# Performance work log

Measured on AMD Instinct MI355X. Metric: run time of the kernel, lower is better.

## Reference

```python
import jax, jax.numpy as jnp
import numpy as np

NUM_USER = 10000
NUM_ITEM = 30000
N = NUM_USER + NUM_ITEM          # total nodes
DIM = 64                          # dim_E == dim_C
E = 500000                        # user-item interactions
NUM_ROUTING = 3
ALPHA_THR = 0.5
NEG_SLOPE_ATTN = 0.2              # GAT attention leaky slope
NEG_SLOPE_ACT = 0.01              # F.leaky_relu_ default


def l2norm(x, eps=1e-12):
    n = jnp.linalg.norm(x, axis=-1, keepdims=True)
    return x / jnp.maximum(n, eps)


def seg_softmax(score, seg):
    # numerically-stable softmax over edges grouped by destination node
    m = jax.ops.segment_max(score, seg, num_segments=N)
    e = jnp.exp(score - m[seg])
    s = jax.ops.segment_sum(e, seg, num_segments=N)
    return e / (s[seg] + 1e-16)


def gat_ori(x, W, src, dst):
    # GATConv_ori: dot-product attention, softmax per destination, scatter-add
    h = x @ W                                     # [N, C]
    score = jax.nn.leaky_relu(jnp.sum(h[dst] * h[src], -1), NEG_SLOPE_ATTN)
    alpha = seg_softmax(score, dst)               # [2E]
    return jax.ops.segment_sum(alpha[:, None] * h[src], dst, num_segments=N)


def gat_pre(x, y, z, W, src, dst):
    # GATConv_pre: primary-modality attention modulated by cross-modal gate (reattn)
    hx = x @ W
    sx = jnp.sum(hx[dst] * hx[src], -1)
    sy = jnp.sum(y[dst] * y[src], -1)
    sz = jnp.sum(z[dst] * z[src], -1)
    alpha = seg_softmax(jax.nn.leaky_relu(sx, NEG_SLOPE_ATTN), dst)
    gate = jax.nn.sigmoid(0.5 * (sy + sz))
    alpha = jnp.where(gate > ALPHA_THR, alpha * gate, alpha)
    return jax.ops.segment_sum(alpha[:, None] * hx[src], dst, num_segments=N)


def cgcn(pref, feat, pref2, feat2, pref3, feat3, src, dst, Wpre, Wori):
    x = jnp.concatenate([pref, feat], 0)
    y = jnp.concatenate([pref2, feat2], 0)
    z = jnp.concatenate([pref3, feat3], 0)
    x = l2norm(gat_pre(x, y, z, Wpre, src, dst))
    for _ in range(NUM_ROUTING):
        x = l2norm(x + gat_ori(x, Wori, src, dst))
    return x


def gcn_conv(x, W, src, dst):
    return jax.ops.segment_sum((x @ W)[src], dst, num_segments=N)


def real_gcn(id_emb, Wg, src, dst):
    x = l2norm(id_emb)
    h1 = jax.nn.leaky_relu(gcn_conv(x, Wg[0], src, dst), NEG_SLOPE_ACT)
    h2 = jax.nn.leaky_relu(gcn_conv(h1, Wg[1], src, dst), NEG_SLOPE_ACT)
    h3 = gcn_conv(h1, Wg[2], src, dst)
    return x + h1 + h2 + h3


def setup_inputs() -> dict:
    key = jax.random.key(0)
    ks = jax.random.split(key, 16)
    users = jax.random.randint(ks[0], (E,), 0, NUM_USER)
    items = jax.random.randint(ks[1], (E,), NUM_USER, N)
    edge_index = jnp.stack([users, items]).astype(jnp.int64)
    s = 0.05
    return {
        'edge_index': edge_index,
        'v_feat': jax.random.normal(ks[2], (NUM_ITEM, 128), jnp.float32),
        'a_feat': jax.random.normal(ks[3], (NUM_ITEM, 128), jnp.float32),
        't_feat': jax.random.normal(ks[4], (NUM_ITEM, 100), jnp.float32),
        'pref_v': jax.random.normal(ks[5], (NUM_USER, DIM), jnp.float32) * s,
        'pref_a': jax.random.normal(ks[6], (NUM_USER, DIM), jnp.float32) * s,
        'pref_t': jax.random.normal(ks[7], (NUM_USER, DIM), jnp.float32) * s,
        'mlp_v_w': jax.random.normal(ks[8], (DIM, 128), jnp.float32) * s,
        'mlp_v_b': jnp.zeros((DIM,), jnp.float32),
        'mlp_a_w': jax.random.normal(ks[9], (DIM, 128), jnp.float32) * s,
        'mlp_a_b': jnp.zeros((DIM,), jnp.float32),
        'mlp_t_w': jax.random.normal(ks[10], (DIM, 100), jnp.float32) * s,
        'mlp_t_b': jnp.zeros((DIM,), jnp.float32),
        'pre_w': jax.random.normal(ks[11], (3, DIM, DIM), jnp.float32) * s,
        'ori_w': jax.random.normal(ks[12], (3, DIM, DIM), jnp.float32) * s,
        'gcn_w': jax.random.normal(ks[13], (3, DIM, DIM), jnp.float32) * s,
        'id_embedding': jax.random.normal(ks[14], (N, DIM), jnp.float32) * s,
    }


def reference(edge_index, v_feat, a_feat, t_feat, pref_v, pref_a, pref_t,
              mlp_v_w, mlp_v_b, mlp_a_w, mlp_a_b, mlp_t_w, mlp_t_b,
              pre_w, ori_w, gcn_w, id_embedding):
    # symmetrize edges (cat with flipped); no self-loops possible (bipartite)
    src = jnp.concatenate([edge_index[0], edge_index[1]])
    dst = jnp.concatenate([edge_index[1], edge_index[0]])

    fv = l2norm(jax.nn.leaky_relu(v_feat @ mlp_v_w.T + mlp_v_b, NEG_SLOPE_ACT))
    fa = l2norm(jax.nn.leaky_relu(a_feat @ mlp_a_w.T + mlp_a_b, NEG_SLOPE_ACT))
    ft = l2norm(jax.nn.leaky_relu(t_feat @ mlp_t_w.T + mlp_t_b, NEG_SLOPE_ACT))
    pv, pa, pt = l2norm(pref_v), l2norm(pref_a), l2norm(pref_t)

    v_rep = cgcn(pv, fv, pa, fa, pt, ft, src, dst, pre_w[0], ori_w[0])
    a_rep = cgcn(pa, fa, pv, fv, pt, ft, src, dst, pre_w[1], ori_w[1])
    t_rep = cgcn(pt, ft, pa, fa, pv, fv, src, dst, pre_w[2], ori_w[2])
    id_rep = real_gcn(id_embedding, gcn_w, src, dst)

    return jnp.concatenate([id_rep, v_rep, a_rep, t_rep], axis=1)  # [N, 4*DIM]
```

## Files before the change

kernel.cpp:

```cpp
#include <hip/hip_runtime.h>
#include <hip/hip_fp16.h>
#include <math.h>

#define NUSER 10000
#define NITEM 30000
#define NN    40000
#define DD    64
#define PLANE ((size_t)NN * DD)

typedef _Float16 hv2 __attribute__((ext_vector_type(2)));
union U2H { unsigned u; hv2 v; __half2 hh; };

#if defined(__has_builtin)
#if __has_builtin(__builtin_amdgcn_fdot2)
#define HAS_FDOT2 1
#endif
#endif

__device__ __forceinline__ float fdot2u(unsigned a, unsigned b, float c) {
#ifdef HAS_FDOT2
    U2H x, y;
    x.u = a;
    y.u = b;
    return __builtin_amdgcn_fdot2(x.v, y.v, c, false);
// ... 53 lines not shown
    __shared__ int wsh[4];
    int b = blockIdx.x, tid = threadIdx.x;
    int base = b * chunk, end = min(n, base + chunk);
    int s = 0;
    for (int i = base + tid; i < end; i += 256) s += cnt[i];
#pragma unroll
    for (int o = 32; o > 0; o >>= 1) s += __shfl_xor(s, o, 64);
    if ((tid & 63) == 0) wsh[tid >> 6] = s;
    __syncthreads();
    if (tid == 0) bsum[b] = wsh[0] + wsh[1] + wsh[2] + wsh[3];
}

__global__ void k_bscan(int* bsum, int nb, int* rp_end) {
    int lane = threadIdx.x;
    int v = (lane < nb) ? bsum[lane] : 0;
    int orig = v;
#pragma unroll
    for (int o = 1; o < 64; o <<= 1) {
        int y = __shfl_up(v, o, 64);
        if (lane >= o) v += y;
    }
    if (lane < nb) bsum[lane] = v - orig;
    if (lane == 63) *rp_end = v;
}

__global__ void k_apply(const int* __restrict__ cnt, const int* __restrict__ boff,
                        int* __restrict__ rp, int n, int chunk) {
    __shared__ int buf[256];
    __shared__ int csh;
    int b = blockIdx.x, tid = threadIdx.x;
    int base = b * chunk, end = min(n, base + chunk);
    int carry = boff[b];
    for (int t0 = base; t0 < end; t0 += 256) {
        int i = t0 + tid;
        int v = (i < end) ? cnt[i] : 0;
        int x = v;
        buf[tid] = x;
        __syncthreads();
        for (int o = 1; o < 256; o <<= 1) {
            int y = (tid >= o) ? buf[tid - o] : 0;
            __syncthreads();
            x += y;
            buf[tid] = x;
            __syncthreads();
        }
        if (i < end) rp[i] = carry + x - v;
        __syncthreads();
        if (tid == 255) csh = carry + x;
        __syncthreads();
        carry = csh;
    }
}

__global__ void k_scatter(const int* ei, int E2, int E, const int* rp, int* fill, int* col) {
    int i = blockIdx.x * blockDim.x + threadIdx.x;
    if (i >= E2) return;
    int j = (i < E) ? i : i - E;
    int s = (i < E) ? ei[j] : ei[E + j];
    int d = (i < E) ? ei[E + j] : ei[j];
    int pos = rp[d] + atomicAdd(&fill[d], 1);
    col[pos] = s;
}

__global__ void k_prep_pref(const float* __restrict__ pv, const float* __restrict__ pa,
                            const float* __restrict__ pt, __half* __restrict__ M) {
    int t = blockIdx.x * blockDim.x + threadIdx.x;
    int w = t >> 6, lane = t & 63, nw = (gridDim.x * blockDim.x) >> 6;
    for (int r = w; r < NUSER; r += nw) {
        float a = pv[(size_t)r * DD + lane];
        float b = pa[(size_t)r * DD + lane];
        float c = pt[(size_t)r * DD + lane];
        float sa = a * a, sb = b * b, sc = c * c;
#pragma unroll
        for (int o = 32; o > 0; o >>= 1) {
            sa += __shfl_xor(sa, o, 64);
            sb += __shfl_xor(sb, o, 64);
            sc += __shfl_xor(sc, o, 64);
        }
        size_t base = (size_t)r * 3 * DD + lane;
        M[base] = __float2half(a / fmaxf(sqrtf(sa), 1e-12f));
        M[base + DD] = __float2half(b / fmaxf(sqrtf(sb), 1e-12f));
        M[base + 2 * DD] = __float2half(c / fmaxf(sqrtf(sc), 1e-12f));
    }
}

template <int K>
__global__ void k_mlp(const float* __restrict__ feat, const float* __restrict__ W,
                      const float* __restrict__ bias, __half* __restrict__ M, int mo) {
    constexpr int K4 = K / 4;
    __shared__ float4 Wl[K4][DD];
    __shared__ float4 rbuf[4][2][K4];
    int t = threadIdx.x, wib = t >> 6, lane = t & 63;
    for (int i = t; i < DD * K4; i += 256) {
        int c = i / K4, k4 = i - c * K4;
        Wl[k4][c] = *(const float4*)(W + (size_t)c * K + k4 * 4);
    }
    __syncthreads();
    float b = bias[lane];
    const int stride = gridDim.x * 4;
    int r = blockIdx.x * 4 + wib;
    float4 v = {0.f, 0.f, 0.f, 0.f};
    if (r < NITEM && lane < K4) v = *(const float4*)(feat + (size_t)r * K + lane * 4);
    int cur = 0;
    for (; r < NITEM; r += stride) {
        if (lane < K4) rbuf[wib][cur][lane] = v;
        int rn = r + stride;
        if (rn < NITEM && lane < K4) v = *(const float4*)(feat + (size_t)rn * K + lane * 4);
        asm volatile("s_waitcnt lgkmcnt(0)" ::: "memory");
        float acc = b;
#pragma unroll
        for (int k4 = 0; k4 < K4; k4++) {
            float4 x4 = rbuf[wib][cur][k4];
            float4 w4 = Wl[k4][lane];
            acc += x4.x * w4.x + x4.y * w4.y + x4.z * w4.z + x4.w * w4.w;
        }
        float h = acc > 0.f ? acc : 0.01f * acc;
        float n = sqrtf(wsum(h * h));
        M[((size_t)(NUSER + r) * 3 + mo) * DD + lane] = __float2half(h / fmaxf(n, 1e-12f));
        cur ^= 1;
    }
}

__global__ void k_gemm_h3(const __half* __restrict__ x3, const float* __restrict__ W3,
                          __half* __restrict__ o3) {
    __shared__ float rowbuf[4][DD];
    int mo = blockIdx.y;
    const float* W = W3 + (size_t)mo * 4096;
    int t = threadIdx.x, wib = t >> 6, lane = t & 63;
    float Wc[DD];
#pragma unroll
    for (int k = 0; k < DD; k++) Wc[k] = W[k * DD + lane];
    for (int r = blockIdx.x * 4 + wib; r < NN; r += gridDim.x * 4) {
        size_t idx = ((size_t)r * 3 + mo) * DD + lane;
        rowbuf[wib][lane] = __half2float(x3[idx]);
        asm volatile("s_waitcnt lgkmcnt(0)" ::: "memory");
        float acc = 0.f;
#pragma unroll
        for (int k4 = 0; k4 < DD / 4; k4++) {
            float4 xq = *(const float4*)&rowbuf[wib][k4 * 4];
            acc += xq.x * Wc[k4 * 4] + xq.y * Wc[k4 * 4 + 1] + xq.z * Wc[k4 * 4 + 2] +
                   xq.w * Wc[k4 * 4 + 3];
        }
        o3[idx] = __float2half(acc);
    }
}

__global__ void k_gemm_f2(const float* __restrict__ x, const float* __restrict__ W2,
                          __half* __restrict__ o2) {
    __shared__ float rowbuf[4][DD];
    int mo = blockIdx.y;
    const float* W = W2 + (size_t)mo * 4096;
    int t = threadIdx.x, wib = t >> 6, lane = t & 63;
    float Wc[DD];
#pragma unroll
    for (int k = 0; k < DD; k++) Wc[k] = W[k * DD + lane];
    for (int r = blockIdx.x * 4 + wib; r < NN; r += gridDim.x * 4) {
        rowbuf[wib][lane] = x[(size_t)r * DD + lane];
        asm volatile("s_waitcnt lgkmcnt(0)" ::: "memory");
        float acc = 0.f;
#pragma unroll
        for (int k4 = 0; k4 < DD / 4; k4++) {
            float4 xq = *(const float4*)&rowbuf[wib][k4 * 4];
            acc += xq.x * Wc[k4 * 4] + xq.y * Wc[k4 * 4 + 1] + xq.z * Wc[k4 * 4 + 2] +
                   xq.w * Wc[k4 * 4 + 3];
        }
        o2[((size_t)r * 2 + mo) * DD + lane] = __float2half(acc);
    }
}

__global__ void k_gemm_id(const float* __restrict__ x, const float* __restrict__ W,
                          __half* __restrict__ hout, float* __restrict__ xnorm) {
    __shared__ float rowbuf[4][DD];
    int t = threadIdx.x, wib = t >> 6, lane = t & 63;
    float Wc[DD];
#pragma unroll
    for (int k = 0; k < DD; k++) Wc[k] = W[k * DD + lane];
    for (int r = blockIdx.x * 4 + wib; r < NN; r += gridDim.x * 4) {
        float xv = x[(size_t)r * DD + lane];
        float n = sqrtf(wsum(xv * xv));
        xv /= fmaxf(n, 1e-12f);
        xnorm[(size_t)r * DD + lane] = xv;
        rowbuf[wib][lane] = xv;
        asm volatile("s_waitcnt lgkmcnt(0)" ::: "memory");
        float acc = 0.f;
#pragma unroll
        for (int k4 = 0; k4 < DD / 4; k4++) {
            float4 xq = *(const float4*)&rowbuf[wib][k4 * 4];
            acc += xq.x * Wc[k4 * 4] + xq.y * Wc[k4 * 4 + 1] + xq.z * Wc[k4 * 4 + 2] +
                   xq.w * Wc[k4 * 4 + 3];
        }
        hout[(size_t)r * DD + lane] = __float2half(acc);
    }
}

__device__ __forceinline__ float gatef(float ssum) {
    float gate = 1.f / (1.f + __expf(-0.5f * ssum));
    return gate > 0.5f ? gate : 1.f;
}

__global__ void k_edgedot3(const __half* __restrict__ M, const int* __restrict__ rp,
                           const int* __restrict__ col, __half* __restrict__ gf4) {
    int t = blockIdx.x * blockDim.x + threadIdx.x;
    int wv = t >> 6, lane = t & 63, nw = (gridDim.x * blockDim.x) >> 6;
    int g = lane >> 3, q = lane & 7;
    for (int w0 = wv; w0 < NN; w0 += nw) {
        int n = nodeperm(w0);
        int e0 = rp[n], e1 = rp[n + 1];
        if (e0 == e1) continue;
        const uint4* trow = (const uint4*)(M + (size_t)n * 192);
        uint4 tv = trow[q], ta = trow[q + 8], tt = trow[q + 16];
        for (int eb = e0 + g; eb < e1; eb += 8) {
            int sn = col[eb];
            const uint4* srow = (const uint4*)(M + (size_t)sn * 192);
            uint4 sv = srow[q], sa = srow[q + 8], st = srow[q + 16];
            float dv = dot8(tv, sv), da = dot8(ta, sa), dt = dot8(tt, st);
            dv = qsum8(dv);
            da = qsum8(da);
            dt = qsum8(dt);
            if (q == 0) {
                U2H p01, p2;
                p01.hh = __floats2half2_rn(gatef(da + dt), gatef(dv + dt));
                p2.hh = __floats2half2_rn(gatef(da + dv), 0.f);
                *(uint2*)(gf4 + (size_t)eb * 4) = make_uint2(p01.u, p2.u);
            }
        }
    }
}

__global__ void k_gat_pre3(const __half* __restrict__ h3, const __half* __restrict__ gf4,
                           const int* __restrict__ rp, const int* __restrict__ col,
                           __half* __restrict__ x3h) {
    int t = blockIdx.x * blockDim.x + threadIdx.x;
    int wv = t >> 6, lane = t & 63, nw = (gridDim.x * blockDim.x) >> 6;
    int g = lane >> 3, q = lane & 7;
    const __half2 z = __floats2half2_rn(0.f, 0.f);
    for (int w0 = wv; w0 < NN; w0 += nw) {
        int n = nodeperm(w0);
        int e0 = rp[n], e1 = rp[n + 1];
        const uint4* hrow = (const uint4*)(h3 + (size_t)n * 192);
        uint4 hd0 = hrow[q], hd1 = hrow[q + 8], hd2 = hrow[q + 16];
        float s0 = 0.f, s1 = 0.f, s2 = 0.f;
        __half2 a0[4] = {z, z, z, z}, a1[4] = {z, z, z, z}, a2[4] = {z, z, z, z};
        for (int eb = e0 + g; eb < e1; eb += 8) {
            int sn = col[eb];
            const uint4* srow = (const uint4*)(h3 + (size_t)sn * 192);
            uint4 v0 = srow[q], v1 = srow[q + 8], v2 = srow[q + 16];
            uint2 gv = *(const uint2*)(gf4 + (size_t)eb * 4);
            float d0 = dot8(hd0, v0), d1 = dot8(hd1, v1), d2 = dot8(hd2, v2);
            d0 = qsum8(d0);
            d1 = qsum8(d1);
            d2 = qsum8(d2);
            float2 g01 = __half22float2(uh(gv.x));
            float g2 = __half22float2(uh(gv.y)).x;
            float sc0 = d0 > 0.f ? d0 : 0.2f * d0;
            float sc1 = d1 > 0.f ? d1 : 0.2f * d1;
            float sc2 = d2 > 0.f ? d2 : 0.2f * d2;
            float p0 = __expf(sc0), p1 = __expf(sc1), p2 = __expf(sc2);
            s0 += p0;
            s1 += p1;
            s2 += p2;
            __half2 ph0 = __float2half2_rn(p0 * g01.x);
            __half2 ph1 = __float2half2_rn(p1 * g01.y);
            __half2 ph2 = __float2half2_rn(p2 * g2);
            a0[0] = __hfma2(ph0, uh(v0.x), a0[0]);
            a0[1] = __hfma2(ph0, uh(v0.y), a0[1]);
            a0[2] = __hfma2(ph0, uh(v0.z), a0[2]);
            a0[3] = __hfma2(ph0, uh(v0.w), a0[3]);
            a1[0] = __hfma2(ph1, uh(v1.x), a1[0]);
            a1[1] = __hfma2(ph1, uh(v1.y), a1[1]);
            a1[2] = __hfma2(ph1, uh(v1.z), a1[2]);
            a1[3] = __hfma2(ph1, uh(v1.w), a1[3]);
            a2[0] = __hfma2(ph2, uh(v2.x), a2[0]);
            a2[1] = __hfma2(ph2, uh(v2.y), a2[1]);
            a2[2] = __hfma2(ph2, uh(v2.z), a2[2]);
            a2[3] = __hfma2(ph2, uh(v2.w), a2[3]);
        }
        s0 = gsum8(s0);
        s1 = gsum8(s1);
        s2 = gsum8(s2);
#pragma unroll
        for (int j = 0; j < 4; j++) {
            a0[j] = h2rx(h2rx(h2rx(a0[j], 8), 16), 32);
            a1[j] = h2rx(h2rx(h2rx(a1[j], 8), 16), 32);
            a2[j] = h2rx(h2rx(h2rx(a2[j], 8), 16), 32);
        }
        float i0 = 1.f / (s0 + 1e-16f), i1 = 1.f / (s1 + 1e-16f), i2 = 1.f / (s2 + 1e-16f);
        float o0[8], o1[8], o2[8];
#pragma unroll
        for (int j = 0; j < 4; j++) {
            float2 f0 = __half22float2(a0[j]);
            float2 f1 = __half22float2(a1[j]);
            float2 f2 = __half22float2(a2[j]);
            o0[2 * j] = f0.x * i0;
            o0[2 * j + 1] = f0.y * i0;
            o1[2 * j] = f1.x * i1;
            o1[2 * j + 1] = f1.y * i1;
            o2[2 * j] = f2.x * i2;
            o2[2 * j + 1] = f2.y * i2;
        }
        float n0 = 0.f, n1 = 0.f, n2 = 0.f;
#pragma unroll
        for (int k = 0; k < 8; k++) {
            n0 += o0[k] * o0[k];
            n1 += o1[k] * o1[k];
            n2 += o2[k] * o2[k];
        }
        n0 = qsum8(n0);
        n1 = qsum8(n1);
        n2 = qsum8(n2);
        float r0 = 1.f / fmaxf(sqrtf(n0), 1e-12f);
        float r1 = 1.f / fmaxf(sqrtf(n1), 1e-12f);
        float r2 = 1.f / fmaxf(sqrtf(n2), 1e-12f);
        if (g == 0) {
            uint4* orow = (uint4*)(x3h + (size_t)n * 192);
            uint4 w0_, w1_, w2_;
            w0_.x = hu(__floats2half2_rn(o0[0] * r0, o0[1] * r0));
            w0_.y = hu(__floats2half2_rn(o0[2] * r0, o0[3] * r0));
            w0_.z = hu(__floats2half2_rn(o0[4] * r0, o0[5] * r0));
            w0_.w = hu(__floats2half2_rn(o0[6] * r0, o0[7] * r0));
            w1_.x = hu(__floats2half2_rn(o1[0] * r1, o1[1] * r1));
            w1_.y = hu(__floats2half2_rn(o1[2] * r1, o1[3] * r1));
            w1_.z = hu(__floats2half2_rn(o1[4] * r1, o1[5] * r1));
            w1_.w = hu(__floats2half2_rn(o1[6] * r1, o1[7] * r1));
            w2_.x = hu(__floats2half2_rn(o2[0] * r2, o2[1] * r2));
            w2_.y = hu(__floats2half2_rn(o2[2] * r2, o2[3] * r2));
            w2_.z = hu(__floats2half2_rn(o2[4] * r2, o2[5] * r2));
            w2_.w = hu(__floats2half2_rn(o2[6] * r2, o2[7] * r2));
            orow[q] = w0_;
            orow[q + 8] = w1_;
            orow[q + 16] = w2_;
        }
    }
}

__global__ void k_gat_ori3(const __half* __restrict__ h3, const __half* __restrict__ x3h,
                           const int* __restrict__ rp, const int* __restrict__ col,
                           __half* __restrict__ xout, float* __restrict__ fout) {
    int t = blockIdx.x * blockDim.x + threadIdx.x;
    int wv = t >> 6, lane = t & 63, nw = (gridDim.x * blockDim.x) >> 6;
    int g = lane >> 3, q = lane & 7;
    const __half2 z = __floats2half2_rn(0.f, 0.f);
    for (int w0 = wv; w0 < NN; w0 += nw) {
        int n = nodeperm(w0);
        int e0 = rp[n], e1 = rp[n + 1];
        const uint4* hrow = (const uint4*)(h3 + (size_t)n * 192);
        uint4 hd0 = hrow[q], hd1 = hrow[q + 8], hd2 = hrow[q + 16];
        float s0 = 0.f, s1 = 0.f, s2 = 0.f;
        __half2 a0[4] = {z, z, z, z}, a1[4] = {z, z, z, z}, a2[4] = {z, z, z, z};
        for (int eb = e0 + g; eb < e1; eb += 8) {
            int sn = col[eb];
            const uint4* srow = (const uint4*)(h3 + (size_t)sn * 192);
            uint4 v0 = srow[q], v1 = srow[q + 8], v2 = srow[q + 16];
            float d0 = dot8(hd0, v0), d1 = dot8(hd1, v1), d2 = dot8(hd2, v2);
            d0 = qsum8(d0);
            d1 = qsum8(d1);
            d2 = qsum8(d2);
            float sc0 = d0 > 0.f ? d0 : 0.2f * d0;
            float sc1 = d1 > 0.f ? d1 : 0.2f * d1;
            float sc2 = d2 > 0.f ? d2 : 0.2f * d2;
            float p0 = __expf(sc0), p1 = __expf(sc1), p2 = __expf(sc2);
            s0 += p0;
            s1 += p1;
            s2 += p2;
            __half2 ph0 = __float2half2_rn(p0);
            __half2 ph1 = __float2half2_rn(p1);
            __half2 ph2 = __float2half2_rn(p2);
            a0[0] = __hfma2(ph0, uh(v0.x), a0[0]);
            a0[1] = __hfma2(ph0, uh(v0.y), a0[1]);
            a0[2] = __hfma2(ph0, uh(v0.z), a0[2]);
            a0[3] = __hfma2(ph0, uh(v0.w), a0[3]);
            a1[0] = __hfma2(ph1, uh(v1.x), a1[0]);
            a1[1] = __hfma2(ph1, uh(v1.y), a1[1]);
            a1[2] = __hfma2(ph1, uh(v1.z), a1[2]);
            a1[3] = __hfma2(ph1, uh(v1.w), a1[3]);
            a2[0] = __hfma2(ph2, uh(v2.x), a2[0]);
            a2[1] = __hfma2(ph2, uh(v2.y), a2[1]);
            a2[2] = __hfma2(ph2, uh(v2.z), a2[2]);
            a2[3] = __hfma2(ph2, uh(v2.w), a2[3]);
        }
        s0 = gsum8(s0);
        s1 = gsum8(s1);
        s2 = gsum8(s2);
#pragma unroll
        for (int j = 0; j < 4; j++) {
            a0[j] = h2rx(h2rx(h2rx(a0[j], 8), 16), 32);
            a1[j] = h2rx(h2rx(h2rx(a1[j], 8), 16), 32);
            a2[j] = h2rx(h2rx(h2rx(a2[j], 8), 16), 32);
        }
        float i0 = 1.f / (s0 + 1e-16f), i1 = 1.f / (s1 + 1e-16f), i2 = 1.f / (s2 + 1e-16f);
        const uint4* xrow = (const uint4*)(x3h + (size_t)n * 192);
        uint4 xr0 = xrow[q], xr1 = xrow[q + 8], xr2 = xrow[q + 16];
        float o0[8], o1[8], o2[8];
#pragma unroll
        for (int j = 0; j < 4; j++) {
            float2 f0 = __half22float2(a0[j]);
            float2 f1 = __half22float2(a1[j]);
            float2 f2 = __half22float2(a2[j]);
            float2 xf0 = __half22float2(uh(j == 0 ? xr0.x : j == 1 ? xr0.y : j == 2 ? xr0.z : xr0.w));
            float2 xf1 = __half22float2(uh(j == 0 ? xr1.x : j == 1 ? xr1.y : j == 2 ? xr1.z : xr1.w));
            float2 xf2 = __half22float2(uh(j == 0 ? xr2.x : j == 1 ? xr2.y : j == 2 ? xr2.z : xr2.w));
            o0[2 * j] = xf0.x + f0.x * i0;
            o0[2 * j + 1] = xf0.y + f0.y * i0;
            o1[2 * j] = xf1.x + f1.x * i1;
            o1[2 * j + 1] = xf1.y + f1.y * i1;
            o2[2 * j] = xf2.x + f2.x * i2;
            o2[2 * j + 1] = xf2.y + f2.y * i2;
        }
        float n0 = 0.f, n1 = 0.f, n2 = 0.f;
#pragma unroll
        for (int k = 0; k < 8; k++) {
            n0 += o0[k] * o0[k];
            n1 += o1[k] * o1[k];
            n2 += o2[k] * o2[k];
        }
        n0 = qsum8(n0);
        n1 = qsum8(n1);
        n2 = qsum8(n2);
        float r0 = 1.f / fmaxf(sqrtf(n0), 1e-12f);
        float r1 = 1.f / fmaxf(sqrtf(n1), 1e-12f);
        float r2 = 1.f / fmaxf(sqrtf(n2), 1e-12f);
        if (g == 0) {
            if (fout) {
                float* ob = fout + (size_t)n * 256 + 64 + q * 8;
                float4 wa, wb;
                wa = make_float4(o0[0] * r0, o0[1] * r0, o0[2] * r0, o0[3] * r0);
                wb = make_float4(o0[4] * r0, o0[5] * r0, o0[6] * r0, o0[7] * r0);
                *(float4*)(ob) = wa;
                *(float4*)(ob + 4) = wb;
                wa = make_float4(o1[0] * r1, o1[1] * r1, o1[2] * r1, o1[3] * r1);
                wb = make_float4(o1[4] * r1, o1[5] * r1, o1[6] * r1, o1[7] * r1);
                *(float4*)(ob + 64) = wa;
                *(float4*)(ob + 68) = wb;
                wa = make_float4(o2[0] * r2, o2[1] * r2, o2[2] * r2, o2[3] * r2);
                wb = make_float4(o2[4] * r2, o2[5] * r2, o2[6] * r2, o2[7] * r2);
                *(float4*)(ob + 128) = wa;
                *(float4*)(ob + 132) = wb;
            } else {
                uint4* orow = (uint4*)(xout + (size_t)n * 192);
                uint4 w0_, w1_, w2_;
                w0_.x = hu(__floats2half2_rn(o0[0] * r0, o0[1] * r0));
                w0_.y = hu(__floats2half2_rn(o0[2] * r0, o0[3] * r0));
                w0_.z = hu(__floats2half2_rn(o0[4] * r0, o0[5] * r0));
                w0_.w = hu(__floats2half2_rn(o0[6] * r0, o0[7] * r0));
                w1_.x = hu(__floats2half2_rn(o1[0] * r1, o1[1] * r1));
                w1_.y = hu(__floats2half2_rn(o1[2] * r1, o1[3] * r1));
                w1_.z = hu(__floats2half2_rn(o1[4] * r1, o1[5] * r1));
                w1_.w = hu(__floats2half2_rn(o1[6] * r1, o1[7] * r1));
                w2_.x = hu(__floats2half2_rn(o2[0] * r2, o2[1] * r2));
                w2_.y = hu(__floats2half2_rn(o2[2] * r2, o2[3] * r2));
                w2_.z = hu(__floats2half2_rn(o2[4] * r2, o2[5] * r2));
                w2_.w = hu(__floats2half2_rn(o2[6] * r2, o2[7] * r2));
                orow[q] = w0_;
                orow[q + 8] = w1_;
                orow[q + 16] = w2_;
            }
        }
    }
}

__global__ void k_gcn1(const __half* __restrict__ h, const int* __restrict__ rp,
                       const int* __restrict__ col, float* __restrict__ out) {
    int t = blockIdx.x * blockDim.x + threadIdx.x;
    int wv = t >> 6, lane = t & 63, nw = (gridDim.x * blockDim.x) >> 6;
    int g = lane >> 3, q = lane & 7;
    const __half2 z = __floats2half2_rn(0.f, 0.f);
    for (int w0 = wv; w0 < NN; w0 += nw) {
        int n = nodeperm(w0);
        int e0 = rp[n], e1 = rp[n + 1];
        __half2 a[4] = {z, z, z, z};
        for (int eb = e0 + g; eb < e1; eb += 8) {
            int sn = col[eb];
            uint4 v = ((const uint4*)(h + (size_t)sn * DD))[q];
            a[0] = __hadd2(a[0], uh(v.x));
            a[1] = __hadd2(a[1], uh(v.y));
            a[2] = __hadd2(a[2], uh(v.z));
            a[3] = __hadd2(a[3], uh(v.w));
        }
#pragma unroll
        for (int j = 0; j < 4; j++) a[j] = h2rx(h2rx(h2rx(a[j], 8), 16), 32);
        if (g == 0) {
            float o[8];
#pragma unroll
            for (int j = 0; j < 4; j++) {
                float2 f = __half22float2(a[j]);
                o[2 * j] = f.x > 0.f ? f.x : 0.01f * f.x;
                o[2 * j + 1] = f.y > 0.f ? f.y : 0.01f * f.y;
            }
            float* ob = out + (size_t)n * DD + q * 8;
            *(float4*)(ob) = make_float4(o[0], o[1], o[2], o[3]);
            *(float4*)(ob + 4) = make_float4(o[4], o[5], o[6], o[7]);
        }
    }
}

__global__ void k_gcn_final2(const __half* __restrict__ gp, const int* __restrict__ rp,
                             const int* __restrict__ col, const float* __restrict__ x0,
                             const float* __restrict__ h1, float* __restrict__ out) {
    int t = blockIdx.x * blockDim.x + threadIdx.x;
    int wv = t >> 6, lane = t & 63, nw = (gridDim.x * blockDim.x) >> 6;
    int g = lane >> 3, q = lane & 7;
    const __half2 z = __floats2half2_rn(0.f, 0.f);
    for (int w0 = wv; w0 < NN; w0 += nw) {
        int n = nodeperm(w0);
        int e0 = rp[n], e1 = rp[n + 1];
        __half2 aA[4] = {z, z, z, z}, aB[4] = {z, z, z, z};
        for (int eb = e0 + g; eb < e1; eb += 8) {
            int sn = col[eb];
// ... 22 lines not shown
#pragma unroll
            for (int j = 0; j < 4; j++) {
                float2 fA = __half22float2(aA[j]);
                float2 fB = __half22float2(aB[j]);
                float h2x = fA.x > 0.f ? fA.x : 0.01f * fA.x;
                float h2y = fA.y > 0.f ? fA.y : 0.01f * fA.y;
                o[2 * j] = h2x + fB.x;
                o[2 * j + 1] = h2y + fB.y;
            }
            float* ob = out + (size_t)n * 256 + q * 8;
            *(float4*)(ob) = make_float4(o[0] + v0a.x + v1a.x, o[1] + v0a.y + v1a.y,
                                         o[2] + v0a.z + v1a.z, o[3] + v0a.w + v1a.w);
            *(float4*)(ob + 4) = make_float4(o[4] + v0b.x + v1b.x, o[5] + v0b.y + v1b.y,
                                             o[6] + v0b.z + v1b.z, o[7] + v0b.w + v1b.w);
        }
    }
}

extern "C" void kernel_launch(void* const* d_in, const int* in_sizes, int n_in,
                              void* d_out, int out_size, void* d_ws, size_t ws_size,
                              hipStream_t stream) {
    const int* ei       = (const int*)d_in[0];
    const float* v_feat = (const float*)d_in[1];
    const float* a_feat = (const float*)d_in[2];
    const float* t_feat = (const float*)d_in[3];
    const float* pref_v = (const float*)d_in[4];
    const float* pref_a = (const float*)d_in[5];
    const float* pref_t = (const float*)d_in[6];
    const float* mlp_v_w = (const float*)d_in[7];
    const float* mlp_v_b = (const float*)d_in[8];
    const float* mlp_a_w = (const float*)d_in[9];
    const float* mlp_a_b = (const float*)d_in[10];
    const float* mlp_t_w = (const float*)d_in[11];
    const float* mlp_t_b = (const float*)d_in[12];
    const float* pre_w  = (const float*)d_in[13];
    const float* ori_w  = (const float*)d_in[14];
    const float* gcn_w  = (const float*)d_in[15];
    const float* id_emb = (const float*)d_in[16];
    float* out = (float*)d_out;

    const int E2 = in_sizes[0];
    const int E  = E2 / 2;

    char* w = (char*)d_ws;
    auto alloc = [&](size_t bytes) -> void* {
        void* p = (void*)w;
        w += (bytes + 255) & ~(size_t)255;
        return p;
    };
    int* cnt  = (int*)alloc((size_t)NN * 4);
    int* rp   = (int*)alloc((size_t)(NN + 1) * 4);
    int* bsum = (int*)alloc(256);
    int* col  = (int*)alloc((size_t)E2 * 4);
    __half* Mh3  = (__half*)alloc(3 * PLANE * 2);
    __half* hb3h = (__half*)alloc(3 * PLANE * 2);
    __half* x3h  = (__half*)alloc(3 * PLANE * 2);
    __half* gf4  = (__half*)alloc((size_t)E2 * 4 * 2);
    float* x0f = (float*)alloc(PLANE * 4);
    float* h1f = (float*)alloc(PLANE * 4);

    __half* g1 = hb3h;
    __half* gpair = hb3h + PLANE;

    const int NBLK = 64, CHUNK = (NN + NBLK - 1) / NBLK;
    hipMemsetAsync(cnt, 0, (size_t)NN * 4, stream);
    k_hist<<<(E2 + 255) / 256, 256, 0, stream>>>(ei, E2, E, cnt);
    k_bsum<<<NBLK, 256, 0, stream>>>(cnt, bsum, NN, CHUNK);
    k_bscan<<<1, 64, 0, stream>>>(bsum, NBLK, rp + NN);
    k_apply<<<NBLK, 256, 0, stream>>>(cnt, bsum, rp, NN, CHUNK);
    hipMemsetAsync(cnt, 0, (size_t)NN * 4, stream);
    k_scatter<<<(E2 + 255) / 256, 256, 0, stream>>>(ei, E2, E, rp, cnt, col);

    k_prep_pref<<<640, 256, 0, stream>>>(pref_v, pref_a, pref_t, Mh3);
    k_mlp<128><<<1024, 256, 0, stream>>>(v_feat, mlp_v_w, mlp_v_b, Mh3, 0);
    k_mlp<128><<<1024, 256, 0, stream>>>(a_feat, mlp_a_w, mlp_a_b, Mh3, 1);
    k_mlp<100><<<1024, 256, 0, stream>>>(t_feat, mlp_t_w, mlp_t_b, Mh3, 2);

    const int GB = (NN + 3) / 4;

    k_edgedot3<<<GB, 256, 0, stream>>>(Mh3, rp, col, gf4);

    dim3 g3(1280, 3);
    k_gemm_h3<<<g3, 256, 0, stream>>>(Mh3, pre_w, hb3h);
    k_gat_pre3<<<GB, 256, 0, stream>>>(hb3h, gf4, rp, col, x3h);
    for (int it = 0; it < 3; it++) {
        k_gemm_h3<<<g3, 256, 0, stream>>>(x3h, ori_w, hb3h);
        if (it < 2)
            k_gat_ori3<<<GB, 256, 0, stream>>>(hb3h, x3h, rp, col, x3h, nullptr);
        else
            k_gat_ori3<<<GB, 256, 0, stream>>>(hb3h, x3h, rp, col, nullptr, out);
    }

    k_gemm_id<<<1280, 256, 0, stream>>>(id_emb, gcn_w, g1, x0f);
    k_gcn1<<<GB, 256, 0, stream>>>(g1, rp, col, h1f);
    dim3 g2(1280, 2);
    k_gemm_f2<<<g2, 256, 0, stream>>>(h1f, gcn_w + 4096, gpair);
    k_gcn_final2<<<GB, 256, 0, stream>>>(gpair, rp, col, x0f, h1f, out);
}
```

Before: 661.5 us.

## Split modality-interleaved node features into planes and run GAT per modality

Changes the feature layout from one interleaved [node][3][64] array to three separate planes. The fused three-modality GAT kernels become single-modality kernels launched once per plane, which shrinks the per-row gather so each plane's working set fits better in cache. The edge dot products are now computed only once per undirected edge, from user nodes, using a new edge-permutation array; they are combined into gates and then expanded to CSR order. The cost is more kernel launches, extra passes over the gate arrays, and no longer sharing col and index loads across modalities.

```diff
diff --git a/kernel.cpp b/kernel.cpp
--- a/kernel.cpp
+++ b/kernel.cpp
@@ -129,7 +129,8 @@
     }
 }
 
-__global__ void k_scatter(const int* ei, int E2, int E, const int* rp, int* fill, int* col) {
+__global__ void k_scatter(const int* ei, int E2, int E, const int* rp, int* fill, int* col,
+                          int* ep) {
     int i = blockIdx.x * blockDim.x + threadIdx.x;
     if (i >= E2) return;
     int j = (i < E) ? i : i - E;
@@ -137,6 +138,7 @@
     int d = (i < E) ? ei[E + j] : ei[j];
     int pos = rp[d] + atomicAdd(&fill[d], 1);
     col[pos] = s;
+    ep[pos] = j;
 }
 
 __global__ void k_prep_pref(const float* __restrict__ pv, const float* __restrict__ pa,
@@ -154,16 +156,16 @@
             sb += __shfl_xor(sb, o, 64);
             sc += __shfl_xor(sc, o, 64);
         }
-        size_t base = (size_t)r * 3 * DD + lane;
+        size_t base = (size_t)r * DD + lane;
         M[base] = __float2half(a / fmaxf(sqrtf(sa), 1e-12f));
-        M[base + DD] = __float2half(b / fmaxf(sqrtf(sb), 1e-12f));
-        M[base + 2 * DD] = __float2half(c / fmaxf(sqrtf(sc), 1e-12f));
+        M[base + PLANE] = __float2half(b / fmaxf(sqrtf(sb), 1e-12f));
+        M[base + 2 * PLANE] = __float2half(c / fmaxf(sqrtf(sc), 1e-12f));
     }
 }
 
 template <int K>
 __global__ void k_mlp(const float* __restrict__ feat, const float* __restrict__ W,
-                      const float* __restrict__ bias, __half* __restrict__ M, int mo) {
+                      const float* __restrict__ bias, __half* __restrict__ Mplane) {
     constexpr int K4 = K / 4;
     __shared__ float4 Wl[K4][DD];
     __shared__ float4 rbuf[4][2][K4];
@@ -193,7 +195,7 @@
         }
         float h = acc > 0.f ? acc : 0.01f * acc;
         float n = sqrtf(wsum(h * h));
-        M[((size_t)(NUSER + r) * 3 + mo) * DD + lane] = __float2half(h / fmaxf(n, 1e-12f));
+        Mplane[(size_t)(NUSER + r) * DD + lane] = __float2half(h / fmaxf(n, 1e-12f));
         cur ^= 1;
     }
 }
@@ -202,14 +204,16 @@
                           __half* __restrict__ o3) {
     __shared__ float rowbuf[4][DD];
     int mo = blockIdx.y;
+    const __half* x = x3 + (size_t)mo * PLANE;
+    __half* o = o3 + (size_t)mo * PLANE;
     const float* W = W3 + (size_t)mo * 4096;
     int t = threadIdx.x, wib = t >> 6, lane = t & 63;
     float Wc[DD];
 #pragma unroll
     for (int k = 0; k < DD; k++) Wc[k] = W[k * DD + lane];
     for (int r = blockIdx.x * 4 + wib; r < NN; r += gridDim.x * 4) {
-        size_t idx = ((size_t)r * 3 + mo) * DD + lane;
-        rowbuf[wib][lane] = __half2float(x3[idx]);
+        size_t idx = (size_t)r * DD + lane;
+        rowbuf[wib][lane] = __half2float(x[idx]);
         asm volatile("s_waitcnt lgkmcnt(0)" ::: "memory");
         float acc = 0.f;
 #pragma unroll
@@ -218,7 +222,7 @@
             acc += xq.x * Wc[k4 * 4] + xq.y * Wc[k4 * 4 + 1] + xq.z * Wc[k4 * 4 + 2] +
                    xq.w * Wc[k4 * 4 + 3];
         }
-        o3[idx] = __float2half(acc);
+        o[idx] = __float2half(acc);
     }
 }
 
@@ -270,43 +274,55 @@
     }
 }
 
+__global__ void k_edgedot_m(const __half* __restrict__ M, const int* __restrict__ rp,
+                            const int* __restrict__ col, const int* __restrict__ ep,
+                            __half* __restrict__ D) {
+    int t = blockIdx.x * blockDim.x + threadIdx.x;
+    int wv = t >> 6, lane = t & 63, nw = (gridDim.x * blockDim.x) >> 6;
+    int g = lane >> 3, q = lane & 7;
+    for (int n = wv; n < NUSER; n += nw) {
+        int e0 = rp[n], e1 = rp[n + 1];
+        uint4 tr = ((const uint4*)(M + (size_t)n * DD))[q];
+        for (int eb = e0 + g; eb < e1; eb += 8) {
+            int sn = col[eb];
+            uint4 sr = ((const uint4*)(M + (size_t)sn * DD))[q];
+            float d = qsum8(dot8(tr, sr));
+            if (q == 0) D[ep[eb]] = __float2half(d);
+        }
+    }
+}
+
 __device__ __forceinline__ float gatef(float ssum) {
     float gate = 1.f / (1.f + __expf(-0.5f * ssum));
     return gate > 0.5f ? gate : 1.f;
 }
 
-__global__ void k_edgedot3(const __half* __restrict__ M, const int* __restrict__ rp,
-                           const int* __restrict__ col, __half* __restrict__ gf4) {
-    int t = blockIdx.x * blockDim.x + threadIdx.x;
-    int wv = t >> 6, lane = t & 63, nw = (gridDim.x * blockDim.x) >> 6;
-    int g = lane >> 3, q = lane & 7;
-    for (int w0 = wv; w0 < NN; w0 += nw) {
-        int n = nodeperm(w0);
-        int e0 = rp[n], e1 = rp[n + 1];
-        if (e0 == e1) continue;
-        const uint4* trow = (const uint4*)(M + (size_t)n * 192);
-        uint4 tv = trow[q], ta = trow[q + 8], tt = trow[q + 16];
-        for (int eb = e0 + g; eb < e1; eb += 8) {
-            int sn = col[eb];
-            const uint4* srow = (const uint4*)(M + (size_t)sn * 192);
-            uint4 sv = srow[q], sa = srow[q + 8], st = srow[q + 16];
-            float dv = dot8(tv, sv), da = dot8(ta, sa), dt = dot8(tt, st);
-            dv = qsum8(dv);
-            da = qsum8(da);
-            dt = qsum8(dt);
-            if (q == 0) {
-                U2H p01, p2;
-                p01.hh = __floats2half2_rn(gatef(da + dt), gatef(dv + dt));
-                p2.hh = __floats2half2_rn(gatef(da + dv), 0.f);
-                *(uint2*)(gf4 + (size_t)eb * 4) = make_uint2(p01.u, p2.u);
-            }
-        }
-    }
-}
-
-__global__ void k_gat_pre3(const __half* __restrict__ h3, const __half* __restrict__ gf4,
-                           const int* __restrict__ rp, const int* __restrict__ col,
-                           __half* __restrict__ x3h) {
+__global__ void k_gatecomb(const __half* __restrict__ Dv, const __half* __restrict__ Da,
+                           const __half* __restrict__ Dt, __half* __restrict__ g0,
+                           __half* __restrict__ g1, __half* __restrict__ g2, int E) {
+    int i = blockIdx.x * blockDim.x + threadIdx.x;
+    if (i >= E) return;
+    float dv = __half2float(Dv[i]), da = __half2float(Da[i]), dt = __half2float(Dt[i]);
+    g0[i] = __float2half(gatef(da + dt));
+    g1[i] = __float2half(gatef(dv + dt));
+    g2[i] = __float2half(gatef(da + dv));
+}
+
+__global__ void k_gateexpand(const int* __restrict__ ep, const __half* __restrict__ g0,
+                             const __half* __restrict__ g1, const __half* __restrict__ g2,
+                             __half* __restrict__ d0, __half* __restrict__ d1,
+                             __half* __restrict__ d2, int E2) {
+    int i = blockIdx.x * blockDim.x + threadIdx.x;
+    if (i >= E2) return;
+    int j = ep[i];
+    d0[i] = g0[j];
+    d1[i] = g1[j];
+    d2[i] = g2[j];
+}
+
+__global__ void k_gat_pre_m(const __half* __restrict__ h, const __half* __restrict__ gfd,
+                            const int* __restrict__ rp, const int* __restrict__ col,
+                            __half* __restrict__ xo) {
     int t = blockIdx.x * blockDim.x + threadIdx.x;
     int wv = t >> 6, lane = t & 63, nw = (gridDim.x * blockDim.x) >> 6;
     int g = lane >> 3, q = lane & 7;
@@ -314,105 +330,53 @@
     for (int w0 = wv; w0 < NN; w0 += nw) {
         int n = nodeperm(w0);
         int e0 = rp[n], e1 = rp[n + 1];
-        const uint4* hrow = (const uint4*)(h3 + (size_t)n * 192);
-        uint4 hd0 = hrow[q], hd1 = hrow[q + 8], hd2 = hrow[q + 16];
-        float s0 = 0.f, s1 = 0.f, s2 = 0.f;
-        __half2 a0[4] = {z, z, z, z}, a1[4] = {z, z, z, z}, a2[4] = {z, z, z, z};
+        uint4 hd = ((const uint4*)(h + (size_t)n * DD))[q];
+        float s = 0.f;
+        __half2 a[4] = {z, z, z, z};
         for (int eb = e0 + g; eb < e1; eb += 8) {
             int sn = col[eb];
-            const uint4* srow = (const uint4*)(h3 + (size_t)sn * 192);
-            uint4 v0 = srow[q], v1 = srow[q + 8], v2 = srow[q + 16];
-            uint2 gv = *(const uint2*)(gf4 + (size_t)eb * 4);
-            float d0 = dot8(hd0, v0), d1 = dot8(hd1, v1), d2 = dot8(hd2, v2);
-            d0 = qsum8(d0);
-            d1 = qsum8(d1);
-            d2 = qsum8(d2);
-            float2 g01 = __half22float2(uh(gv.x));
-            float g2 = __half22float2(uh(gv.y)).x;
-            float sc0 = d0 > 0.f ? d0 : 0.2f * d0;
-            float sc1 = d1 > 0.f ? d1 : 0.2f * d1;
-            float sc2 = d2 > 0.f ? d2 : 0.2f * d2;
-            float p0 = __expf(sc0), p1 = __expf(sc1), p2 = __expf(sc2);
-            s0 += p0;
-            s1 += p1;
-            s2 += p2;
-            __half2 ph0 = __float2half2_rn(p0 * g01.x);
-            __half2 ph1 = __float2half2_rn(p1 * g01.y);
-            __half2 ph2 = __float2half2_rn(p2 * g2);
-            a0[0] = __hfma2(ph0, uh(v0.x), a0[0]);
-            a0[1] = __hfma2(ph0, uh(v0.y), a0[1]);
-            a0[2] = __hfma2(ph0, uh(v0.z), a0[2]);
-            a0[3] = __hfma2(ph0, uh(v0.w), a0[3]);
-            a1[0] = __hfma2(ph1, uh(v1.x), a1[0]);
-            a1[1] = __hfma2(ph1, uh(v1.y), a1[1]);
-            a1[2] = __hfma2(ph1, uh(v1.z), a1[2]);
-            a1[3] = __hfma2(ph1, uh(v1.w), a1[3]);
-            a2[0] = __hfma2(ph2, uh(v2.x), a2[0]);
-            a2[1] = __hfma2(ph2, uh(v2.y), a2[1]);
-            a2[2] = __hfma2(ph2, uh(v2.z), a2[2]);
-            a2[3] = __hfma2(ph2, uh(v2.w), a2[3]);
-        }
-        s0 = gsum8(s0);
-        s1 = gsum8(s1);
-        s2 = gsum8(s2);
+            uint4 v = ((const uint4*)(h + (size_t)sn * DD))[q];
+            float d = qsum8(dot8(hd, v));
+            float gt = __half2float(gfd[eb]);
+            float sc = d > 0.f ? d : 0.2f * d;
+            float p = __expf(sc);
+            s += p;
+            __half2 pg = __float2half2_rn(p * gt);
+            a[0] = __hfma2(pg, uh(v.x), a[0]);
+            a[1] = __hfma2(pg, uh(v.y), a[1]);
+            a[2] = __hfma2(pg, uh(v.z), a[2]);
+            a[3] = __hfma2(pg, uh(v.w), a[3]);
+        }
+        s = gsum8(s);
+#pragma unroll
+        for (int j = 0; j < 4; j++) a[j] = h2rx(h2rx(h2rx(a[j], 8), 16), 32);
+        float i0 = 1.f / (s + 1e-16f);
+        float o[8];
 #pragma unroll
         for (int j = 0; j < 4; j++) {
-            a0[j] = h2rx(h2rx(h2rx(a0[j], 8), 16), 32);
-            a1[j] = h2rx(h2rx(h2rx(a1[j], 8), 16), 32);
-            a2[j] = h2rx(h2rx(h2rx(a2[j], 8), 16), 32);
-        }
-        float i0 = 1.f / (s0 + 1e-16f), i1 = 1.f / (s1 + 1e-16f), i2 = 1.f / (s2 + 1e-16f);
-        float o0[8], o1[8], o2[8];
-#pragma unroll
-        for (int j = 0; j < 4; j++) {
-            float2 f0 = __half22float2(a0[j]);
-            float2 f1 = __half22float2(a1[j]);
-            float2 f2 = __half22float2(a2[j]);
-            o0[2 * j] = f0.x * i0;
-            o0[2 * j + 1] = f0.y * i0;
-            o1[2 * j] = f1.x * i1;
-            o1[2 * j + 1] = f1.y * i1;
-            o2[2 * j] = f2.x * i2;
-            o2[2 * j + 1] = f2.y * i2;
-        }
-        float n0 = 0.f, n1 = 0.f, n2 = 0.f;
-#pragma unroll
-        for (int k = 0; k < 8; k++) {
-            n0 += o0[k] * o0[k];
-            n1 += o1[k] * o1[k];
-            n2 += o2[k] * o2[k];
-        }
+            float2 f = __half22float2(a[j]);
+            o[2 * j] = f.x * i0;
+            o[2 * j + 1] = f.y * i0;
+        }
+        float n0 = 0.f;
+#pragma unroll
+        for (int k = 0; k < 8; k++) n0 += o[k] * o[k];
         n0 = qsum8(n0);
-        n1 = qsum8(n1);
-        n2 = qsum8(n2);
         float r0 = 1.f / fmaxf(sqrtf(n0), 1e-12f);
-        float r1 = 1.f / fmaxf(sqrtf(n1), 1e-12f);
-        float r2 = 1.f / fmaxf(sqrtf(n2), 1e-12f);
         if (g == 0) {
-            uint4* orow = (uint4*)(x3h + (size_t)n * 192);
-            uint4 w0_, w1_, w2_;
-            w0_.x = hu(__floats2half2_rn(o0[0] * r0, o0[1] * r0));
-            w0_.y = hu(__floats2half2_rn(o0[2] * r0, o0[3] * r0));
-            w0_.z = hu(__floats2half2_rn(o0[4] * r0, o0[5] * r0));
-            w0_.w = hu(__floats2half2_rn(o0[6] * r0, o0[7] * r0));
-            w1_.x = hu(__floats2half2_rn(o1[0] * r1, o1[1] * r1));
-            w1_.y = hu(__floats2half2_rn(o1[2] * r1, o1[3] * r1));
-            w1_.z = hu(__floats2half2_rn(o1[4] * r1, o1[5] * r1));
-            w1_.w = hu(__floats2half2_rn(o1[6] * r1, o1[7] * r1));
-            w2_.x = hu(__floats2half2_rn(o2[0] * r2, o2[1] * r2));
-            w2_.y = hu(__floats2half2_rn(o2[2] * r2, o2[3] * r2));
-            w2_.z = hu(__floats2half2_rn(o2[4] * r2, o2[5] * r2));
-            w2_.w = hu(__floats2half2_rn(o2[6] * r2, o2[7] * r2));
-            orow[q] = w0_;
-            orow[q + 8] = w1_;
-            orow[q + 16] = w2_;
-        }
-    }
-}
-
-__global__ void k_gat_ori3(const __half* __restrict__ h3, const __half* __restrict__ x3h,
-                           const int* __restrict__ rp, const int* __restrict__ col,
-                           __half* __restrict__ xout, float* __restrict__ fout) {
+            uint4 w_;
+            w_.x = hu(__floats2half2_rn(o[0] * r0, o[1] * r0));
+            w_.y = hu(__floats2half2_rn(o[2] * r0, o[3] * r0));
+            w_.z = hu(__floats2half2_rn(o[4] * r0, o[5] * r0));
+            w_.w = hu(__floats2half2_rn(o[6] * r0, o[7] * r0));
+            ((uint4*)(xo + (size_t)n * DD))[q] = w_;
+        }
+    }
+}
+
+__global__ void k_gat_ori_m(const __half* __restrict__ h, const __half* __restrict__ xin,
+                            const int* __restrict__ rp, const int* __restrict__ col,
+                            __half* __restrict__ xout, float* __restrict__ fout) {
     int t = blockIdx.x * blockDim.x + threadIdx.x;
     int wv = t >> 6, lane = t & 63, nw = (gridDim.x * blockDim.x) >> 6;
     int g = lane >> 3, q = lane & 7;
@@ -420,116 +384,52 @@
     for (int w0 = wv; w0 < NN; w0 += nw) {
         int n = nodeperm(w0);
         int e0 = rp[n], e1 = rp[n + 1];
-        const uint4* hrow = (const uint4*)(h3 + (size_t)n * 192);
-        uint4 hd0 = hrow[q], hd1 = hrow[q + 8], hd2 = hrow[q + 16];
-        float s0 = 0.f, s1 = 0.f, s2 = 0.f;
-        __half2 a0[4] = {z, z, z, z}, a1[4] = {z, z, z, z}, a2[4] = {z, z, z, z};
+        uint4 hd = ((const uint4*)(h + (size_t)n * DD))[q];
+        float s = 0.f;
+        __half2 a[4] = {z, z, z, z};
         for (int eb = e0 + g; eb < e1; eb += 8) {
             int sn = col[eb];
-            const uint4* srow = (const uint4*)(h3 + (size_t)sn * 192);
-            uint4 v0 = srow[q], v1 = srow[q + 8], v2 = srow[q + 16];
-            float d0 = dot8(hd0, v0), d1 = dot8(hd1, v1), d2 = dot8(hd2, v2);
-            d0 = qsum8(d0);
-            d1 = qsum8(d1);
-            d2 = qsum8(d2);
-            float sc0 = d0 > 0.f ? d0 : 0.2f * d0;
-            float sc1 = d1 > 0.f ? d1 : 0.2f * d1;
-            float sc2 = d2 > 0.f ? d2 : 0.2f * d2;
-            float p0 = __expf(sc0), p1 = __expf(sc1), p2 = __expf(sc2);
-            s0 += p0;
-            s1 += p1;
-            s2 += p2;
-            __half2 ph0 = __float2half2_rn(p0);
-            __half2 ph1 = __float2half2_rn(p1);
-            __half2 ph2 = __float2half2_rn(p2);
-            a0[0] = __hfma2(ph0, uh(v0.x), a0[0]);
-            a0[1] = __hfma2(ph0, uh(v0.y), a0[1]);
-            a0[2] = __hfma2(ph0, uh(v0.z), a0[2]);
-            a0[3] = __hfma2(ph0, uh(v0.w), a0[3]);
-            a1[0] = __hfma2(ph1, uh(v1.x), a1[0]);
-            a1[1] = __hfma2(ph1, uh(v1.y), a1[1]);
-            a1[2] = __hfma2(ph1, uh(v1.z), a1[2]);
-            a1[3] = __hfma2(ph1, uh(v1.w), a1[3]);
-            a2[0] = __hfma2(ph2, uh(v2.x), a2[0]);
-            a2[1] = __hfma2(ph2, uh(v2.y), a2[1]);
-            a2[2] = __hfma2(ph2, uh(v2.z), a2[2]);
-            a2[3] = __hfma2(ph2, uh(v2.w), a2[3]);
-        }
-        s0 = gsum8(s0);
-        s1 = gsum8(s1);
-        s2 = gsum8(s2);
+            uint4 v = ((const uint4*)(h + (size_t)sn * DD))[q];
+            float d = qsum8(dot8(hd, v));
+            float sc = d > 0.f ? d : 0.2f * d;
+            float p = __expf(sc);
+            s += p;
+            __half2 ph = __float2half2_rn(p);
+            a[0] = __hfma2(ph, uh(v.x), a[0]);
+            a[1] = __hfma2(ph, uh(v.y), a[1]);
+            a[2] = __hfma2(ph, uh(v.z), a[2]);
+            a[3] = __hfma2(ph, uh(v.w), a[3]);
+        }
+        s = gsum8(s);
+#pragma unroll
+        for (int j = 0; j < 4; j++) a[j] = h2rx(h2rx(h2rx(a[j], 8), 16), 32);
+        float i0 = 1.f / (s + 1e-16f);
+        uint4 xr = ((const uint4*)(xin + (size_t)n * DD))[q];
+        float o[8];
 #pragma unroll
         for (int j = 0; j < 4; j++) {
-            a0[j] = h2rx(h2rx(h2rx(a0[j], 8), 16), 32);
-            a1[j] = h2rx(h2rx(h2rx(a1[j], 8), 16), 32);
-            a2[j] = h2rx(h2rx(h2rx(a2[j], 8), 16), 32);
-        }
-        float i0 = 1.f / (s0 + 1e-16f), i1 = 1.f / (s1 + 1e-16f), i2 = 1.f / (s2 + 1e-16f);
-        const uint4* xrow = (const uint4*)(x3h + (size_t)n * 192);
-        uint4 xr0 = xrow[q], xr1 = xrow[q + 8], xr2 = xrow[q + 16];
-        float o0[8], o1[8], o2[8];
-#pragma unroll
-        for (int j = 0; j < 4; j++) {
-            float2 f0 = __half22float2(a0[j]);
-            float2 f1 = __half22float2(a1[j]);
-            float2 f2 = __half22float2(a2[j]);
-            float2 xf0 = __half22float2(uh(j == 0 ? xr0.x : j == 1 ? xr0.y : j == 2 ? xr0.z : xr0.w));
-            float2 xf1 = __half22float2(uh(j == 0 ? xr1.x : j == 1 ? xr1.y : j == 2 ? xr1.z : xr1.w));
-            float2 xf2 = __half22float2(uh(j == 0 ? xr2.x : j == 1 ? xr2.y : j == 2 ? xr2.z : xr2.w));
-            o0[2 * j] = xf0.x + f0.x * i0;
-            o0[2 * j + 1] = xf0.y + f0.y * i0;
-            o1[2 * j] = xf1.x + f1.x * i1;
-            o1[2 * j + 1] = xf1.y + f1.y * i1;
-            o2[2 * j] = xf2.x + f2.x * i2;
-            o2[2 * j + 1] = xf2.y + f2.y * i2;
-        }
-        float n0 = 0.f, n1 = 0.f, n2 = 0.f;
-#pragma unroll
-        for (int k = 0; k < 8; k++) {
-            n0 += o0[k] * o0[k];
-            n1 += o1[k] * o1[k];
-            n2 += o2[k] * o2[k];
-        }
+            float2 f = __half22float2(a[j]);
+            float2 xf = __half22float2(uh(j == 0 ? xr.x : j == 1 ? xr.y : j == 2 ? xr.z : xr.w));
+            o[2 * j] = xf.x + f.x * i0;
+            o[2 * j + 1] = xf.y + f.y * i0;
+        }
+        float n0 = 0.f;
+#pragma unroll
+        for (int k = 0; k < 8; k++) n0 += o[k] * o[k];
         n0 = qsum8(n0);
-        n1 = qsum8(n1);
-        n2 = qsum8(n2);
         float r0 = 1.f / fmaxf(sqrtf(n0), 1e-12f);
-        float r1 = 1.f / fmaxf(sqrtf(n1), 1e-12f);
-        float r2 = 1.f / fmaxf(sqrtf(n2), 1e-12f);
         if (g == 0) {
             if (fout) {
-                float* ob = fout + (size_t)n * 256 + 64 + q * 8;
-                float4 wa, wb;
-                wa = make_float4(o0[0] * r0, o0[1] * r0, o0[2] * r0, o0[3] * r0);
-                wb = make_float4(o0[4] * r0, o0[5] * r0, o0[6] * r0, o0[7] * r0);
-                *(float4*)(ob) = wa;
-                *(float4*)(ob + 4) = wb;
-                wa = make_float4(o1[0] * r1, o1[1] * r1, o1[2] * r1, o1[3] * r1);
-                wb = make_float4(o1[4] * r1, o1[5] * r1, o1[6] * r1, o1[7] * r1);
-                *(float4*)(ob + 64) = wa;
-                *(float4*)(ob + 68) = wb;
-                wa = make_float4(o2[0] * r2, o2[1] * r2, o2[2] * r2, o2[3] * r2);
-                wb = make_float4(o2[4] * r2, o2[5] * r2, o2[6] * r2, o2[7] * r2);
-                *(float4*)(ob + 128) = wa;
-                *(float4*)(ob + 132) = wb;
+                float* ob = fout + (size_t)n * 256 + q * 8;
+                *(float4*)(ob) = make_float4(o[0] * r0, o[1] * r0, o[2] * r0, o[3] * r0);
+                *(float4*)(ob + 4) = make_float4(o[4] * r0, o[5] * r0, o[6] * r0, o[7] * r0);
             } else {
-                uint4* orow = (uint4*)(xout + (size_t)n * 192);
-                uint4 w0_, w1_, w2_;
-                w0_.x = hu(__floats2half2_rn(o0[0] * r0, o0[1] * r0));
-                w0_.y = hu(__floats2half2_rn(o0[2] * r0, o0[3] * r0));
-                w0_.z = hu(__floats2half2_rn(o0[4] * r0, o0[5] * r0));
-                w0_.w = hu(__floats2half2_rn(o0[6] * r0, o0[7] * r0));
-                w1_.x = hu(__floats2half2_rn(o1[0] * r1, o1[1] * r1));
-                w1_.y = hu(__floats2half2_rn(o1[2] * r1, o1[3] * r1));
-                w1_.z = hu(__floats2half2_rn(o1[4] * r1, o1[5] * r1));
-                w1_.w = hu(__floats2half2_rn(o1[6] * r1, o1[7] * r1));
-                w2_.x = hu(__floats2half2_rn(o2[0] * r2, o2[1] * r2));
-                w2_.y = hu(__floats2half2_rn(o2[2] * r2, o2[3] * r2));
-                w2_.z = hu(__floats2half2_rn(o2[4] * r2, o2[5] * r2));
-                w2_.w = hu(__floats2half2_rn(o2[6] * r2, o2[7] * r2));
-                orow[q] = w0_;
-                orow[q + 8] = w1_;
-                orow[q + 16] = w2_;
+                uint4 w_;
+                w_.x = hu(__floats2half2_rn(o[0] * r0, o[1] * r0));
+                w_.y = hu(__floats2half2_rn(o[2] * r0, o[3] * r0));
+                w_.z = hu(__floats2half2_rn(o[4] * r0, o[5] * r0));
+                w_.w = hu(__floats2half2_rn(o[6] * r0, o[7] * r0));
+                ((uint4*)(xout + (size_t)n * DD))[q] = w_;
             }
         }
     }
@@ -658,15 +558,18 @@
     int* rp   = (int*)alloc((size_t)(NN + 1) * 4);
     int* bsum = (int*)alloc(256);
     int* col  = (int*)alloc((size_t)E2 * 4);
-    __half* Mh3  = (__half*)alloc(3 * PLANE * 2);
-    __half* hb3h = (__half*)alloc(3 * PLANE * 2);
-    __half* x3h  = (__half*)alloc(3 * PLANE * 2);
-    __half* gf4  = (__half*)alloc((size_t)E2 * 4 * 2);
+    int* ep   = (int*)alloc((size_t)E2 * 4);
+    __half* Mh  = (__half*)alloc(3 * PLANE * 2);
+    __half* hb  = (__half*)alloc(3 * PLANE * 2);
+    __half* x3h = (__half*)alloc(3 * PLANE * 2);
+    __half* Dm  = (__half*)alloc((size_t)3 * E * 2);
+    __half* gfp = (__half*)alloc((size_t)3 * E * 2);
+    __half* gfd = (__half*)alloc((size_t)3 * E2 * 2);
     float* x0f = (float*)alloc(PLANE * 4);
     float* h1f = (float*)alloc(PLANE * 4);
 
-    __half* g1 = hb3h;
-    __half* gpair = hb3h + PLANE;
+    __half* g1 = hb;
+    __half* gpair = hb + PLANE;
 
     const int NBLK = 64, CHUNK = (NN + NBLK - 1) / NBLK;
     hipMemsetAsync(cnt, 0, (size_t)NN * 4, stream);
@@ -675,26 +578,40 @@
     k_bscan<<<1, 64, 0, stream>>>(bsum, NBLK, rp + NN);
     k_apply<<<NBLK, 256, 0, stream>>>(cnt, bsum, rp, NN, CHUNK);
     hipMemsetAsync(cnt, 0, (size_t)NN * 4, stream);
-    k_scatter<<<(E2 + 255) / 256, 256, 0, stream>>>(ei, E2, E, rp, cnt, col);
-
-    k_prep_pref<<<640, 256, 0, stream>>>(pref_v, pref_a, pref_t, Mh3);
-    k_mlp<128><<<1024, 256, 0, stream>>>(v_feat, mlp_v_w, mlp_v_b, Mh3, 0);
-    k_mlp<128><<<1024, 256, 0, stream>>>(a_feat, mlp_a_w, mlp_a_b, Mh3, 1);
-    k_mlp<100><<<1024, 256, 0, stream>>>(t_feat, mlp_t_w, mlp_t_b, Mh3, 2);
+    k_scatter<<<(E2 + 255) / 256, 256, 0, stream>>>(ei, E2, E, rp, cnt, col, ep);
+
+    k_prep_pref<<<640, 256, 0, stream>>>(pref_v, pref_a, pref_t, Mh);
+    k_mlp<128><<<1024, 256, 0, stream>>>(v_feat, mlp_v_w, mlp_v_b, Mh);
+    k_mlp<128><<<1024, 256, 0, stream>>>(a_feat, mlp_a_w, mlp_a_b, Mh + PLANE);
+    k_mlp<100><<<1024, 256, 0, stream>>>(t_feat, mlp_t_w, mlp_t_b, Mh + 2 * PLANE);
 
     const int GB = (NN + 3) / 4;
-
-    k_edgedot3<<<GB, 256, 0, stream>>>(Mh3, rp, col, gf4);
+    const int UB = (NUSER + 3) / 4;
+
+    k_edgedot_m<<<UB, 256, 0, stream>>>(Mh, rp, col, ep, Dm);
+    k_edgedot_m<<<UB, 256, 0, stream>>>(Mh + PLANE, rp, col, ep, Dm + E);
+    k_edgedot_m<<<UB, 256, 0, stream>>>(Mh + 2 * PLANE, rp, col, ep, Dm + 2 * (size_t)E);
+    k_gatecomb<<<(E + 255) / 256, 256, 0, stream>>>(Dm, Dm + E, Dm + 2 * (size_t)E, gfp,
+                                                    gfp + E, gfp + 2 * (size_t)E, E);
+    k_gateexpand<<<(E2 + 255) / 256, 256, 0, stream>>>(ep, gfp, gfp + E, gfp + 2 * (size_t)E,
+                                                       gfd, gfd + E2, gfd + 2 * (size_t)E2, E2);
 
     dim3 g3(1280, 3);
-    k_gemm_h3<<<g3, 256, 0, stream>>>(Mh3, pre_w, hb3h);
-    k_gat_pre3<<<GB, 256, 0, stream>>>(hb3h, gf4, rp, col, x3h);
+    k_gemm_h3<<<g3, 256, 0, stream>>>(Mh, pre_w, hb);
+    for (int mo = 0; mo < 3; mo++)
+        k_gat_pre_m<<<GB, 256, 0, stream>>>(hb + (size_t)mo * PLANE, gfd + (size_t)mo * E2, rp,
+                                            col, x3h + (size_t)mo * PLANE);
     for (int it = 0; it < 3; it++) {
-        k_gemm_h3<<<g3, 256, 0, stream>>>(x3h, ori_w, hb3h);
-        if (it < 2)
-            k_gat_ori3<<<GB, 256, 0, stream>>>(hb3h, x3h, rp, col, x3h, nullptr);
-        else
-            k_gat_ori3<<<GB, 256, 0, stream>>>(hb3h, x3h, rp, col, nullptr, out);
+        k_gemm_h3<<<g3, 256, 0, stream>>>(x3h, ori_w, hb);
+        for (int mo = 0; mo < 3; mo++) {
+            __half* hp = hb + (size_t)mo * PLANE;
+            __half* xp = x3h + (size_t)mo * PLANE;
+            if (it < 2)
+                k_gat_ori_m<<<GB, 256, 0, stream>>>(hp, xp, rp, col, xp, nullptr);
+            else
+                k_gat_ori_m<<<GB, 256, 0, stream>>>(hp, xp, rp, col, nullptr,
+                                                    out + 64 + mo * 64);
+        }
     }
 
     k_gemm_id<<<1280, 256, 0, stream>>>(id_emb, gcn_w, g1, x0f);
```

Result: slower. 825.0 us (+24.7%).
